# Performance work log

Measured on AMD Instinct MI355X. Metric: run time of the kernel, lower is better.

## Reference

```python
import jax, jax.numpy as jnp
import numpy as np

N, E = 40000, 640000
DIN, HID, H = 512, 128, 4
C = HID  # per-head channels; H*C == 512 == DIN
BN_EPS = 1e-5


def setup_inputs() -> dict:
    key = jax.random.key(0)
    ks = jax.random.split(key, 32)
    sc = 0.05
    d = {}
    d["x"] = jax.random.normal(ks[0], (N, DIN), jnp.float32)
    d["edge_index"] = jax.random.randint(ks[1], (2, E), 0, N)
    i = 2
    for l in (1, 2, 3):
        d[f"W{l}"] = jax.random.normal(ks[i], (DIN, H * C), jnp.float32) * sc; i += 1
        d[f"as{l}"] = jax.random.normal(ks[i], (H, C), jnp.float32) * sc; i += 1
        d[f"ad{l}"] = jax.random.normal(ks[i], (H, C), jnp.float32) * sc; i += 1
        d[f"b{l}"] = jnp.zeros((H * C,), jnp.float32)
        d[f"g{l}"] = jnp.ones((H * C,), jnp.float32)
        d[f"be{l}"] = jnp.zeros((H * C,), jnp.float32)
    d["Wg1"] = jax.random.normal(ks[i], (H * C, HID), jnp.float32) * sc; i += 1
    d["bg1"] = jnp.zeros((HID,), jnp.float32)
    d["Wg2"] = jax.random.normal(ks[i], (HID, 1), jnp.float32) * sc; i += 1
    d["bg2"] = jnp.zeros((1,), jnp.float32)
    d["Wf1"] = jax.random.normal(ks[i], (H * C, HID), jnp.float32) * sc; i += 1
    d["bf1"] = jnp.zeros((HID,), jnp.float32)
    d["Wf2"] = jax.random.normal(ks[i], (HID, HID), jnp.float32) * sc; i += 1
    d["bf2"] = jnp.zeros((HID,), jnp.float32)
    d["Wp"] = jax.random.normal(ks[i], (HID + H * C, HID), jnp.float32) * sc; i += 1
    d["bp"] = jnp.zeros((HID,), jnp.float32)
    return d


def _gat(x, src, dst, W, a_s, a_d, b):
    # PyG GATConv (concat=True, negative_slope=0.2, self-loops already in src/dst)
    n = x.shape[0]
    h = (x @ W).reshape(n, H, C)                      # [N,H,C]
    es = jnp.einsum('nhc,hc->nh', h, a_s)             # alpha_src per node
    ed = jnp.einsum('nhc,hc->nh', h, a_d)             # alpha_dst per node
    e = jax.nn.leaky_relu(es[src] + ed[dst], 0.2)     # [Etot,H]
    m = jax.ops.segment_max(e, dst, num_segments=n)   # softmax over incoming edges
    ex = jnp.exp(e - m[dst])
    s = jax.ops.segment_sum(ex, dst, num_segments=n)
    w = ex / (s[dst] + 1e-16)                         # [Etot,H]
    out = jax.ops.segment_sum(w[:, :, None] * h[src], dst, num_segments=n)
    return out.reshape(n, H * C) + b


def _bn(x, g, b):
    mu = x.mean(0)
    var = x.var(0)
    return (x - mu) * jax.lax.rsqrt(var + BN_EPS) * g + b


def reference(x, edge_index,
              W1, as1, ad1, b1, g1, be1,
              W2, as2, ad2, b2, g2, be2,
              W3, as3, ad3, b3, g3, be3,
              Wg1, bg1, Wg2, bg2, Wf1, bf1, Wf2, bf2, Wp, bp):
    n = x.shape[0]
    loops = jnp.arange(n)
    src = jnp.concatenate([edge_index[0], loops])
    dst = jnp.concatenate([edge_index[1], loops])

    h = jax.nn.leaky_relu(_bn(_gat(x, src, dst, W1, as1, ad1, b1), g1, be1), 0.2)
    h_res = h
    h = jax.nn.leaky_relu(_bn(_gat(h, src, dst, W2, as2, ad2, b2), g2, be2), 0.2) + h_res
    h_res = h
    h = jax.nn.leaky_relu(_bn(_gat(h, src, dst, W3, as3, ad3, b3), g3, be3), 0.2) + h_res

    attn_scores = (jnp.tanh(h @ Wg1 + bg1) @ Wg2 + bg2)[:, 0]   # [N]
    attn_w = jax.nn.softmax(attn_scores)                        # softmax over all nodes
    feat = jax.nn.relu(h @ Wf1 + bf1) @ Wf2 + bf2               # [N,HID]
    gated = (attn_w[:, None] * feat).sum(0)                     # [HID]
    global_pooled = h.mean(0, keepdims=True)                    # batch=None -> one graph
    combined = jnp.concatenate([gated[None, :], global_pooled], axis=-1)  # [1,640]
    out = (combined @ Wp + bp)[0]                               # [HID]
    return out, attn_scores
```

## Files before the change

kernel.cpp:

```cpp
#include <hip/hip_runtime.h>
#include <math.h>

#define N_NODES 40000
#define M_PAD   40064
#define N_EDGES 640000
#define ETOT    (N_EDGES + N_NODES)
#define DINC    512
#define NHEAD   4
#define CHD     128
#define BN_EPS  1e-5f

typedef __attribute__((ext_vector_type(8))) short bf16x8;
typedef __attribute__((ext_vector_type(4))) float f32x4;

static __device__ __forceinline__ float lrelu(float x) { return x > 0.f ? x : 0.2f * x; }

static __device__ __forceinline__ unsigned short f2b(float f) {
    union { float f; unsigned int u; } v; v.f = f;
    unsigned int r = (v.u + 0x7fff + ((v.u >> 16) & 1)) >> 16;
    return (unsigned short)r;
}
static __device__ __forceinline__ float b2f(unsigned short b) {
    union { unsigned int u; float f; } v; v.u = ((unsigned int)b) << 16;
    return v.f;
}
static __device__ __forceinline__ float lo16(unsigned int u) {
    union { unsigned int u; float f; } v; v.u = u << 16; return v.f;
}
static __device__ __forceinline__ float hi16(unsigned int u) {
    union { unsigned int u; float f; } v; v.u = u & 0xffff0000u; return v.f;
}

static __device__ __forceinline__ void fma8(float* acc, uint4 hv, float wgt) {
    acc[0] += wgt * lo16(hv.x); acc[1] += wgt * hi16(hv.x);
    acc[2] += wgt * lo16(hv.y); acc[3] += wgt * hi16(hv.y);
    acc[4] += wgt * lo16(hv.z); acc[5] += wgt * hi16(hv.z);
    acc[6] += wgt * lo16(hv.w); acc[7] += wgt * hi16(hv.w);
}

#define GLDS16(g, l) __builtin_amdgcn_global_load_lds( \
    (__attribute__((address_space(1))) void*)(g),      \
    (__attribute__((address_space(3))) void*)(l), 16, 0, 0)

#define CVTX_BLK 10000
__global__ __launch_bounds__(256) void k_prep(const float4* __restrict__ xin,
                                              uint4* __restrict__ xb,
                                              uint4* __restrict__ curb,
                                              uint4* __restrict__ cnt4) {
    int bid = blockIdx.x;
    int tid = threadIdx.x;
    if (bid < CVTX_BLK) {
        size_t i = (size_t)bid * 256 + tid;
        float4 a = xin[i * 2], b = xin[i * 2 + 1];
        uint4 o;
        o.x = (unsigned)f2b(a.x) | ((unsigned)f2b(a.y) << 16);
        o.y = (unsigned)f2b(a.z) | ((unsigned)f2b(a.w) << 16);
        o.z = (unsigned)f2b(b.x) | ((unsigned)f2b(b.y) << 16);
        o.w = (unsigned)f2b(b.z) | ((unsigned)f2b(b.w) << 16);
        xb[i] = o;
    } else if (bid < CVTX_BLK + 16) {
        int i = (bid - CVTX_BLK) * 256 + tid;
        xb[(size_t)N_NODES * DINC / 8 + i] = make_uint4(0, 0, 0, 0);
    } else if (bid < CVTX_BLK + 32) {
        int i = (bid - CVTX_BLK - 16) * 256 + tid;
        curb[(size_t)N_NODES * DINC / 8 + i] = make_uint4(0, 0, 0, 0);
    } else {
        int i = (bid - CVTX_BLK - 32) * 256 + tid;
        if (i < N_NODES / 4) cnt4[i] = make_uint4(0, 0, 0, 0);
    }
}

__global__ __launch_bounds__(256) void k_cvtw_all(const float* __restrict__ W1, unsigned short* __restrict__ T1,
                                                  const float* __restrict__ W2, unsigned short* __restrict__ T2,
                                                  const float* __restrict__ W3, unsigned short* __restrict__ T3,
                                                  const float* __restrict__ Wg1, const float* __restrict__ Wf1,
                                                  unsigned short* __restrict__ Wct) {
    int idx = blockIdx.x * 256 + threadIdx.x;
    const float* W; unsigned short* T; int Nn;
    if (idx < 262144)            { W = W1; T = T1; Nn = 512; }
    else if (idx < 524288)       { W = W2; T = T2; Nn = 512; idx -= 262144; }
    else if (idx < 786432)       { W = W3; T = T3; Nn = 512; idx -= 524288; }
    else if (idx < 851968)       { W = Wg1; T = Wct; Nn = 128; idx -= 786432; }
    else                         { W = Wf1; T = Wct + 65536; Nn = 128; idx -= 851968; }
    int k = idx / Nn, n = idx % Nn;
    T[(size_t)n * 512 + k] = f2b(W[idx]);
}

__global__ void k_degree(const int* __restrict__ ei, int* __restrict__ cnt) {
    int e = blockIdx.x * 256 + threadIdx.x;
    if (e < ETOT) {
        int dst = (e < N_EDGES) ? ei[N_EDGES + e] : (e - N_EDGES);
        atomicAdd(&cnt[dst], 1);
    }
}

__global__ __launch_bounds__(64) void k_scan1(const int* __restrict__ deg, int* __restrict__ bsum) {
    int lane = threadIdx.x;
    int v = deg[blockIdx.x * 64 + lane];
#pragma unroll
    for (int off = 32; off; off >>= 1) v += __shfl_xor(v, off);
    if (lane == 0) bsum[blockIdx.x] = v;
}

__global__ __launch_bounds__(64) void k_scan23(const int* __restrict__ deg, const int* __restrict__ bsum,
                                               int* __restrict__ rowptr, int* __restrict__ cnt) {
    int b = blockIdx.x, lane = threadIdx.x;
    int pre = 0;
    for (int i = lane; i < b; i += 64) pre += bsum[i];
#pragma unroll
    for (int off = 32; off; off >>= 1) pre += __shfl_xor(pre, off);
    int i = b * 64 + lane;
    int v = deg[i];
    int inc = v;
#pragma unroll
    for (int off = 1; off < 64; off <<= 1) {
        int t = __shfl_up(inc, off);
        if (lane >= off) inc += t;
    }
    rowptr[i] = pre + inc - v;
    cnt[i] = 0;
    if (b == 624 && lane == 63) rowptr[N_NODES] = ETOT;
}

__global__ void k_fill(const int* __restrict__ ei, const int* __restrict__ rowptr,
                       int* __restrict__ cnt, int* __restrict__ csr_src) {
    int e = blockIdx.x * 256 + threadIdx.x;
    if (e < ETOT) {
        int src, dst;
        if (e < N_EDGES) { src = ei[e]; dst = ei[N_EDGES + e]; }
        else             { src = e - N_EDGES; dst = src; }
        int pos = rowptr[dst] + atomicAdd(&cnt[dst], 1);
        csr_src[pos] = src;
    }
}

template<int CBF16, int EPI>
__global__ __launch_bounds__(256) void k_gemm_mfma(const unsigned short* __restrict__ A,
                                                   const unsigned short* __restrict__ Bt,
                                                   void* __restrict__ Cout,
                                                   int Nn, int K, int nbn,
                                                   const float* __restrict__ p1,
                                                   const float* __restrict__ p2,
                                                   float* __restrict__ p3,
                                                   float* __restrict__ p4,
                                                   const float* __restrict__ p5,
                                                   const float* __restrict__ p6) {
    __shared__ alignas(16) unsigned short As[128 * 64];
    __shared__ alignas(16) unsigned short Bs[128 * 64];
    const int tid  = threadIdx.x;
    const int wv   = tid >> 6;
    const int lane = tid & 63;
    const int bm = (blockIdx.x / nbn) * 128;
    const int bn = (blockIdx.x % nbn) * 128;
    const int wm = (wv >> 1) * 64;
    const int wn = (wv & 1) * 64;

    const int srow = lane >> 3;
    const int scol = (((lane & 7) ^ srow) * 8);
    const size_t a_base = (size_t)(bm + wv * 32 + srow) * K + scol;
    const size_t b_base = (size_t)(bn + wv * 32 + srow) * K + scol;

    f32x4 acc[4][4] = {};

    for (int k0 = 0; k0 < K; k0 += 64) {
#pragma unroll
        for (int q = 0; q < 4; ++q)
            GLDS16(A + a_base + (size_t)q * 8 * K + k0, &As[(wv * 32 + q * 8) * 64]);
#pragma unroll
        for (int q = 0; q < 4; ++q)
            GLDS16(Bt + b_base + (size_t)q * 8 * K + k0, &Bs[(wv * 32 + q * 8) * 64]);
        __syncthreads();

        const int r0 = lane & 15;
#pragma unroll
        for (int ks = 0; ks < 2; ++ks) {
            const int c = ks * 4 + (lane >> 4);
            bf16x8 af[4], bfr[4];
#pragma unroll
            for (int i = 0; i < 4; ++i) {
                int row = wm + i * 16 + r0;
                af[i] = *(const bf16x8*)&As[row * 64 + ((c ^ (row & 7)) * 8)];
            }
#pragma unroll
            for (int j = 0; j < 4; ++j) {
                int row = wn + j * 16 + r0;
                bfr[j] = *(const bf16x8*)&Bs[row * 64 + ((c ^ (row & 7)) * 8)];
            }
#pragma unroll
            for (int i = 0; i < 4; ++i)
#pragma unroll
                for (int j = 0; j < 4; ++j)
                    acc[i][j] = __builtin_amdgcn_mfma_f32_16x16x32_bf16(af[i], bfr[j], acc[i][j], 0, 0, 0);
        }
        __syncthreads();
    }

    const int crow0 = bm + wm + (lane >> 4) * 4;
    const int ccol  = bn + wn + (lane & 15);

    if (EPI != 2) {
#pragma unroll
        for (int i = 0; i < 4; ++i)
#pragma unroll
            for (int j = 0; j < 4; ++j)
#pragma unroll
                for (int r = 0; r < 4; ++r) {
                    size_t off = (size_t)(crow0 + i * 16 + r) * Nn + ccol + j * 16;
                    if (CBF16) ((unsigned short*)Cout)[off] = f2b(acc[i][j][r]);
                    else       ((float*)Cout)[off] = acc[i][j][r];
                }
    }

    if (EPI == 1) {
        const int head = bn >> 7;
        float asv[4], adv[4];
#pragma unroll
        for (int j = 0; j < 4; ++j) {
            int cc = head * CHD + wn + j * 16 + (lane & 15);
            asv[j] = p1[cc];
            adv[j] = p2[cc];
        }
        float* sE = (float*)As;
        sE[tid] = 0.f;
        __syncthreads();
#pragma unroll
        for (int i = 0; i < 4; ++i)
#pragma unroll
            for (int r = 0; r < 4; ++r) {
                float e = acc[i][0][r] * asv[0] + acc[i][1][r] * asv[1]
                        + acc[i][2][r] * asv[2] + acc[i][3][r] * asv[3];
                float d = acc[i][0][r] * adv[0] + acc[i][1][r] * adv[1]
                        + acc[i][2][r] * adv[2] + acc[i][3][r] * adv[3];
#pragma unroll
                for (int off = 8; off; off >>= 1) {
                    e += __shfl_xor(e, off);
                    d += __shfl_xor(d, off);
                }
                if ((lane & 15) == 0) {
                    int rloc = wm + i * 16 + (lane >> 4) * 4 + r;
                    atomicAdd(&sE[rloc], e);
                    atomicAdd(&sE[128 + rloc], d);
                }
            }
        __syncthreads();
        if (tid < 128) {
            p3[(size_t)(bm + tid) * NHEAD + head] = sE[tid];
            p4[(size_t)(bm + tid) * NHEAD + head] = sE[128 + tid];
        }
    }

    if (EPI == 2) {
        if (bn == 0) {
            float wgv[4], bgv[4];
#pragma unroll
            for (int j = 0; j < 4; ++j) {
                int cc = wn + j * 16 + (lane & 15);
                bgv[j] = p1[cc];
                wgv[j] = p2[cc];
            }
            float* sE = (float*)As;
            sE[tid] = 0.f;
            __syncthreads();
#pragma unroll
            for (int i = 0; i < 4; ++i)
#pragma unroll
                for (int r = 0; r < 4; ++r) {
                    float e = tanhf(acc[i][0][r] + bgv[0]) * wgv[0]
                            + tanhf(acc[i][1][r] + bgv[1]) * wgv[1]
                            + tanhf(acc[i][2][r] + bgv[2]) * wgv[2]
                            + tanhf(acc[i][3][r] + bgv[3]) * wgv[3];
#pragma unroll
                    for (int off = 8; off; off >>= 1) e += __shfl_xor(e, off);
                    if ((lane & 15) == 0)
                        atomicAdd(&sE[wm + i * 16 + (lane >> 4) * 4 + r], e);
                }
            __syncthreads();
            if (tid < 128) p3[bm + tid] = sE[tid] + p5[0];
        } else {
#pragma unroll
            for (int j = 0; j < 4; ++j) {
                int colF = wn + j * 16 + (lane & 15);
                float bv = p6[colF];
#pragma unroll
                for (int i = 0; i < 4; ++i)
#pragma unroll
                    for (int r = 0; r < 4; ++r)
                        p4[(size_t)(crow0 + i * 16 + r) * 128 + colF] =
                            fmaxf(acc[i][j][r] + bv, 0.f);
            }
        }
    }
}

__global__ __launch_bounds__(256) void k_wts(const float4* __restrict__ es4,
                                             const float4* __restrict__ ed4,
                                             const int* __restrict__ rowptr,
                                             const int* __restrict__ csr_src,
                                             float4* __restrict__ wbuf4,
                                             float4* __restrict__ inv4,
                                             float* __restrict__ stats) {
    if (blockIdx.x == 0)
        for (int q = threadIdx.x; q < DINC * 2; q += 256) stats[q] = 0.f;
    int n = blockIdx.x * 4 + (threadIdx.x >> 6);
    int lane = threadIdx.x & 63;
    int start = rowptr[n], end = rowptr[n + 1];
    float4 edn = ed4[n];
    float4 mx = make_float4(-1e30f, -1e30f, -1e30f, -1e30f);
    for (int j0 = start; j0 < end; j0 += 64) {
        int j = j0 + lane;
        if (j < end) {
            int s = csr_src[j];
            float4 e = es4[s];
            mx.x = fmaxf(mx.x, lrelu(e.x + edn.x));
            mx.y = fmaxf(mx.y, lrelu(e.y + edn.y));
            mx.z = fmaxf(mx.z, lrelu(e.z + edn.z));
            mx.w = fmaxf(mx.w, lrelu(e.w + edn.w));
        }
    }
#pragma unroll
    for (int off = 32; off; off >>= 1) {
        mx.x = fmaxf(mx.x, __shfl_xor(mx.x, off));
        mx.y = fmaxf(mx.y, __shfl_xor(mx.y, off));
        mx.z = fmaxf(mx.z, __shfl_xor(mx.z, off));
        mx.w = fmaxf(mx.w, __shfl_xor(mx.w, off));
    }
    float4 sum = make_float4(0.f, 0.f, 0.f, 0.f);
    for (int j0 = start; j0 < end; j0 += 64) {
        int j = j0 + lane;
        if (j < end) {
            int s = csr_src[j];
            float4 e = es4[s];
            float4 ex;
            ex.x = __expf(lrelu(e.x + edn.x) - mx.x);
            ex.y = __expf(lrelu(e.y + edn.y) - mx.y);
            ex.z = __expf(lrelu(e.z + edn.z) - mx.z);
            ex.w = __expf(lrelu(e.w + edn.w) - mx.w);
            wbuf4[j] = ex;
            sum.x += ex.x; sum.y += ex.y; sum.z += ex.z; sum.w += ex.w;
        }
    }
#pragma unroll
    for (int off = 32; off; off >>= 1) {
        sum.x += __shfl_xor(sum.x, off);
        sum.y += __shfl_xor(sum.y, off);
        sum.z += __shfl_xor(sum.z, off);
        sum.w += __shfl_xor(sum.w, off);
    }
    if (lane == 0) {
        float4 iv;
        iv.x = 1.f / (sum.x + 1e-16f);
        iv.y = 1.f / (sum.y + 1e-16f);
        iv.z = 1.f / (sum.z + 1e-16f);
        iv.w = 1.f / (sum.w + 1e-16f);
        inv4[n] = iv;
    }
}

__global__ __launch_bounds__(256) void k_agg(const unsigned short* __restrict__ hb,
                                             const int* __restrict__ rowptr,
                                             const int* __restrict__ csr_src,
                                             const float* __restrict__ wbuf,
                                             const float* __restrict__ invp,
                                             unsigned short* __restrict__ aggb) {
    __shared__ float part[4][512];
    const int n = blockIdx.x;
    const int tid = threadIdx.x;
    const int grp = tid >> 6;
    const int lane = tid & 63;
    const int head = lane >> 4;
    const int start = rowptr[n], end = rowptr[n + 1];

    float acc[8] = {};
    int j = start + grp;
    int s_n = 0; float w_n = 0.f;
    if (j < end) { s_n = csr_src[j]; w_n = wbuf[j * 4 + head]; }
    while (j < end) {
        int s = s_n; float wgt = w_n;
        int j2 = j + 4;
        if (j2 < end) { s_n = csr_src[j2]; w_n = wbuf[j2 * 4 + head]; }
        uint4 hv = *(const uint4*)&hb[(size_t)s * DINC + lane * 8];
        fma8(acc, hv, wgt);
        j = j2;
    }
    *(float4*)&part[grp][lane * 8]     = make_float4(acc[0], acc[1], acc[2], acc[3]);
    *(float4*)&part[grp][lane * 8 + 4] = make_float4(acc[4], acc[5], acc[6], acc[7]);
    __syncthreads();
    const int c = tid * 2;
    float v0 = part[0][c] + part[1][c] + part[2][c] + part[3][c];
    float v1 = part[0][c + 1] + part[1][c + 1] + part[2][c + 1] + part[3][c + 1];
    float iv = invp[(n << 2) + (c >> 7)];
    v0 *= iv; v1 *= iv;
    unsigned int o = (unsigned)f2b(v0) | ((unsigned)f2b(v1) << 16);
    *(unsigned int*)&aggb[(size_t)n * DINC + c] = o;
}

__global__ __launch_bounds__(256) void k_bn_stats(const unsigned short* __restrict__ aggb,
                                                  float* __restrict__ stats) {
    int tid = threadIdx.x;
    int row0 = blockIdx.x * 64;
    int c0 = tid * 2;
    float s0 = 0, q0 = 0, s1 = 0, q1 = 0;
    for (int r = row0; r < row0 + 64; ++r) {
        unsigned int hv = *(const unsigned int*)&aggb[(size_t)r * DINC + c0];
        float v0 = lo16(hv), v1 = hi16(hv);
        s0 += v0; q0 += v0 * v0;
        s1 += v1; q1 += v1 * v1;
    }
    atomicAdd(&stats[c0], s0);
    atomicAdd(&stats[c0 + 1], s1);
    atomicAdd(&stats[DINC + c0], q0);
    atomicAdd(&stats[DINC + c0 + 1], q1);
}

__global__ __launch_bounds__(256) void k_bn_act(const unsigned short* __restrict__ aggb,
                                                const float* __restrict__ stats,
                                                const float* __restrict__ g,
                                                const float* __restrict__ be,
                                                unsigned short* __restrict__ curb,
                                                int res) {
    size_t idx = (size_t)blockIdx.x * 256 + threadIdx.x;
    int c8 = ((int)(idx & 63)) * 8;
    uint4 v = *(const uint4*)&aggb[idx * 8];
    float xv[8] = { lo16(v.x), hi16(v.x), lo16(v.y), hi16(v.y),
                    lo16(v.z), hi16(v.z), lo16(v.w), hi16(v.w) };
#pragma unroll
    for (int q = 0; q < 8; ++q) {
        int c = c8 + q;
        float mu = stats[c] * (1.f / N_NODES);
        float var = stats[DINC + c] * (1.f / N_NODES) - mu * mu;
        float A = g[c] * rsqrtf(var + BN_EPS);
        float B = be[c] - mu * A;
        xv[q] = lrelu(xv[q] * A + B);
    }
    if (res) {
        uint4 r = *(const uint4*)&curb[idx * 8];
        xv[0] += lo16(r.x); xv[1] += hi16(r.x);
        xv[2] += lo16(r.y); xv[3] += hi16(r.y);
        xv[4] += lo16(r.z); xv[5] += hi16(r.z);
        xv[6] += lo16(r.w); xv[7] += hi16(r.w);
    }
    uint4 o;
    o.x = (unsigned)f2b(xv[0]) | ((unsigned)f2b(xv[1]) << 16);
    o.y = (unsigned)f2b(xv[2]) | ((unsigned)f2b(xv[3]) << 16);
    o.z = (unsigned)f2b(xv[4]) | ((unsigned)f2b(xv[5]) << 16);
    o.w = (unsigned)f2b(xv[6]) | ((unsigned)f2b(xv[7]) << 16);
    *(uint4*)&curb[idx * 8] = o;
}

__global__ __launch_bounds__(1024) void k_softmax(const float* __restrict__ scores, float* __restrict__ sm,
                                                  float* __restrict__ vbuf, float* __restrict__ pooled) {
    __shared__ float red[16];
    int tid = threadIdx.x, lane = tid & 63, wv = tid >> 6;
    if (tid < 128) vbuf[tid] = 0.f;
    if (tid < DINC) pooled[tid] = 0.f;
    float m = -1e30f;
    for (int i = tid; i < N_NODES; i += 1024) m = fmaxf(m, scores[i]);
#pragma unroll
    for (int off = 32; off; off >>= 1) m = fmaxf(m, __shfl_xor(m, off));
    if (lane == 0) red[wv] = m;
    __syncthreads();
    float mall = red[0];
    for (int i = 1; i < 16; ++i) mall = fmaxf(mall, red[i]);
    __syncthreads();
    float s = 0.f;
    for (int i = tid; i < N_NODES; i += 1024) s += expf(scores[i] - mall);
#pragma unroll
    for (int off = 32; off; off >>= 1) s += __shfl_xor(s, off);
    if (lane == 0) red[wv] = s;
    __syncthreads();
    if (tid == 0) {
        float tot = 0.f;
        for (int i = 0; i < 16; ++i) tot += red[i];
        sm[0] = mall; sm[1] = tot;
    }
}

__global__ __launch_bounds__(640) void k_vpool(const float* __restrict__ Fb,
                                               const unsigned short* __restrict__ hb,
                                               const float* __restrict__ scores,
                                               const float* __restrict__ sm,
                                               float* __restrict__ v,
                                               float* __restrict__ pooled) {
    int tid = threadIdx.x;
    int row0 = blockIdx.x * 64;
    float mall = sm[0];
    float invS = 1.f / sm[1];
    if (tid < 128) {
        float acc = 0.f;
        for (int r = row0; r < row0 + 64; ++r) {
            float w = expf(scores[r] - mall) * invS;
            acc += w * Fb[(size_t)r * 128 + tid];
        }
        atomicAdd(&v[tid], acc);
    } else {
        int c = tid - 128;
        float acc = 0.f;
        for (int r = row0; r < row0 + 64; ++r) acc += b2f(hb[(size_t)r * DINC + c]);
        atomicAdd(&pooled[c], acc * (1.f / N_NODES));
    }
}

__global__ __launch_bounds__(128) void k_final(const float* __restrict__ v,
                                               const float* __restrict__ pooled,
                                               const float* __restrict__ Wf2,
                                               const float* __restrict__ bf2,
                                               const float* __restrict__ Wp,
                                               const float* __restrict__ bp,
                                               float* __restrict__ out) {
    __shared__ float sg[128];
    int o = threadIdx.x;
    float g = bf2[o];
    for (int k = 0; k < 128; ++k) g += v[k] * Wf2[k * 128 + o];
    sg[o] = g;
    __syncthreads();
    float acc = bp[o];
    for (int c = 0; c < 128; ++c) acc += sg[c] * Wp[c * 128 + o];
    for (int j = 0; j < 512; ++j) acc += pooled[j] * Wp[(128 + j) * 128 + o];
    out[o] = acc;
}

extern "C" void kernel_launch(void* const* d_in, const int* in_sizes, int n_in,
                              void* d_out, int out_size, void* d_ws, size_t ws_size,
                              hipStream_t stream) {
    const float* x  = (const float*)d_in[0];
    const int*   ei = (const int*)d_in[1];
    const float* Wg1 = (const float*)d_in[20];
    const float* bg1 = (const float*)d_in[21];
    const float* Wg2 = (const float*)d_in[22];
    const float* bg2 = (const float*)d_in[23];
    const float* Wf1 = (const float*)d_in[24];
    const float* bf1 = (const float*)d_in[25];
    const float* Wf2 = (const float*)d_in[26];
    const float* bf2 = (const float*)d_in[27];
    const float* Wp  = (const float*)d_in[28];
    const float* bp  = (const float*)d_in[29];
    float* out = (float*)d_out;

    char* base = (char*)d_ws;
    size_t off = 0;
    auto take = [&](size_t nbytes) -> char* {
        char* p = base + off;
        off += (nbytes + 255) & ~(size_t)255;
        return p;
    };
    unsigned short* hb   = (unsigned short*)take((size_t)M_PAD * DINC * 2);
    unsigned short* curb = (unsigned short*)take((size_t)M_PAD * DINC * 2);
    unsigned short* xb   = (unsigned short*)take((size_t)M_PAD * DINC * 2);
    unsigned short* aggb = (unsigned short*)take((size_t)M_PAD * DINC * 2);
    float* Fb    = (float*)take((size_t)M_PAD * 128 * 4);
    float* es    = (float*)take((size_t)M_PAD * NHEAD * 4);
    float* ed    = (float*)take((size_t)M_PAD * NHEAD * 4);
    float* wbuf  = (float*)take((size_t)ETOT * NHEAD * 4);
    float* invp  = (float*)take((size_t)N_NODES * NHEAD * 4);
    int*   rowptr= (int*)take((size_t)(N_NODES + 1) * 4);
    int*   cnt   = (int*)take((size_t)N_NODES * 4);
    int*   csr   = (int*)take((size_t)ETOT * 4);
    int*   bsum  = (int*)take(625 * 4);
    float* stats = (float*)take(DINC * 2 * 4);
    float* sm    = (float*)take(2 * 4);
    float* vbuf  = (float*)take(128 * 4);
    float* pooled= (float*)take(DINC * 4);
    unsigned short* Wt1  = (unsigned short*)take((size_t)DINC * DINC * 2);
    unsigned short* Wt2  = (unsigned short*)take((size_t)DINC * DINC * 2);
    unsigned short* Wt3  = (unsigned short*)take((size_t)DINC * DINC * 2);
    unsigned short* Wct  = (unsigned short*)take((size_t)256 * DINC * 2);

    k_prep<<<CVTX_BLK + 32 + 40, 256, 0, stream>>>((const float4*)x, (uint4*)xb,
                                                   (uint4*)curb, (uint4*)cnt);
    k_cvtw_all<<<3584, 256, 0, stream>>>((const float*)d_in[2], Wt1,
                                         (const float*)d_in[8], Wt2,
                                         (const float*)d_in[14], Wt3,
                                         Wg1, Wf1, Wct);
    k_degree<<<(ETOT + 255) / 256, 256, 0, stream>>>(ei, cnt);
    k_scan1<<<625, 64, 0, stream>>>(cnt, bsum);
    k_scan23<<<625, 64, 0, stream>>>(cnt, bsum, rowptr, cnt);
    k_fill<<<(ETOT + 255) / 256, 256, 0, stream>>>(ei, rowptr, cnt, csr);

    const unsigned short* Wts[3] = {Wt1, Wt2, Wt3};
    const unsigned short* in = xb;
    for (int l = 0; l < 3; ++l) {
        const float* as_ = (const float*)d_in[2 + l * 6 + 1];
        const float* ad_ = (const float*)d_in[2 + l * 6 + 2];
        const float* g   = (const float*)d_in[2 + l * 6 + 4];
        const float* be  = (const float*)d_in[2 + l * 6 + 5];

        k_gemm_mfma<1, 1><<<(M_PAD / 128) * (DINC / 128), 256, 0, stream>>>(
            in, Wts[l], hb, DINC, DINC, DINC / 128, as_, ad_, es, ed, nullptr, nullptr);
        k_wts<<<N_NODES / 4, 256, 0, stream>>>((const float4*)es, (const float4*)ed, rowptr, csr,
                                               (float4*)wbuf, (float4*)invp, stats);
        k_agg<<<N_NODES, 256, 0, stream>>>(hb, rowptr, csr, wbuf, invp, aggb);
        k_bn_stats<<<N_NODES / 64, 256, 0, stream>>>(aggb, stats);
        k_bn_act<<<(N_NODES * (DINC / 8)) / 256, 256, 0, stream>>>(aggb, stats, g, be, curb, l > 0 ? 1 : 0);
        in = curb;
    }

    float* scores = out + 128;
    k_gemm_mfma<0, 2><<<(M_PAD / 128) * 2, 256, 0, stream>>>(
        curb, Wct, nullptr, 256, DINC, 2, bg1, Wg2, scores, Fb, bg2, bf1);

    k_softmax<<<1, 1024, 0, stream>>>(scores, sm, vbuf, pooled);
    k_vpool<<<N_NODES / 64, 640, 0, stream>>>(Fb, curb, scores, sm, vbuf, pooled);
    k_final<<<1, 128, 0, stream>>>(vbuf, pooled, Wf2, bf2, Wp, bp, out);
}
```

Baseline: 891.6 us.

## Fuse edge softmax weight computation into aggregation kernel and drop max pass

Removes the separate k_wts kernel. Each aggregation block now computes exp of the leaky-relu edge logits directly into shared memory and accumulates per-head sums with shared atomics, eliminating the global wbuf/invp round trip and one launch per layer. The max-subtraction pass is dropped, relying on softmax shift invariance, which risks overflow for large logits. The pooling kernel is also narrowed to 384 threads, each reading two bf16 columns per load.

```diff
diff --git a/kernel.cpp b/kernel.cpp
--- a/kernel.cpp
+++ b/kernel.cpp
@@ -292,77 +292,17 @@
     }
 }
 
-__global__ __launch_bounds__(256) void k_wts(const float4* __restrict__ es4,
+__global__ __launch_bounds__(256) void k_agg(const unsigned short* __restrict__ hb,
+                                             const float4* __restrict__ es4,
                                              const float4* __restrict__ ed4,
                                              const int* __restrict__ rowptr,
                                              const int* __restrict__ csr_src,
-                                             float4* __restrict__ wbuf4,
-                                             float4* __restrict__ inv4,
+                                             unsigned short* __restrict__ aggb,
                                              float* __restrict__ stats) {
-    if (blockIdx.x == 0)
-        for (int q = threadIdx.x; q < DINC * 2; q += 256) stats[q] = 0.f;
-    int n = blockIdx.x * 4 + (threadIdx.x >> 6);
-    int lane = threadIdx.x & 63;
-    int start = rowptr[n], end = rowptr[n + 1];
-    float4 edn = ed4[n];
-    float4 mx = make_float4(-1e30f, -1e30f, -1e30f, -1e30f);
-    for (int j0 = start; j0 < end; j0 += 64) {
-        int j = j0 + lane;
-        if (j < end) {
-            int s = csr_src[j];
-            float4 e = es4[s];
-            mx.x = fmaxf(mx.x, lrelu(e.x + edn.x));
-            mx.y = fmaxf(mx.y, lrelu(e.y + edn.y));
-            mx.z = fmaxf(mx.z, lrelu(e.z + edn.z));
-            mx.w = fmaxf(mx.w, lrelu(e.w + edn.w));
-        }
-    }
-#pragma unroll
-    for (int off = 32; off; off >>= 1) {
-        mx.x = fmaxf(mx.x, __shfl_xor(mx.x, off));
-        mx.y = fmaxf(mx.y, __shfl_xor(mx.y, off));
-        mx.z = fmaxf(mx.z, __shfl_xor(mx.z, off));
-        mx.w = fmaxf(mx.w, __shfl_xor(mx.w, off));
-    }
-    float4 sum = make_float4(0.f, 0.f, 0.f, 0.f);
-    for (int j0 = start; j0 < end; j0 += 64) {
-        int j = j0 + lane;
-        if (j < end) {
-            int s = csr_src[j];
-            float4 e = es4[s];
-            float4 ex;
-            ex.x = __expf(lrelu(e.x + edn.x) - mx.x);
-            ex.y = __expf(lrelu(e.y + edn.y) - mx.y);
-            ex.z = __expf(lrelu(e.z + edn.z) - mx.z);
-            ex.w = __expf(lrelu(e.w + edn.w) - mx.w);
-            wbuf4[j] = ex;
-            sum.x += ex.x; sum.y += ex.y; sum.z += ex.z; sum.w += ex.w;
-        }
-    }
-#pragma unroll
-    for (int off = 32; off; off >>= 1) {
-        sum.x += __shfl_xor(sum.x, off);
-        sum.y += __shfl_xor(sum.y, off);
-        sum.z += __shfl_xor(sum.z, off);
-        sum.w += __shfl_xor(sum.w, off);
-    }
-    if (lane == 0) {
-        float4 iv;
-        iv.x = 1.f / (sum.x + 1e-16f);
-        iv.y = 1.f / (sum.y + 1e-16f);
-        iv.z = 1.f / (sum.z + 1e-16f);
-        iv.w = 1.f / (sum.w + 1e-16f);
-        inv4[n] = iv;
-    }
-}
-
-__global__ __launch_bounds__(256) void k_agg(const unsigned short* __restrict__ hb,
-                                             const int* __restrict__ rowptr,
-                                             const int* __restrict__ csr_src,
-                                             const float* __restrict__ wbuf,
-                                             const float* __restrict__ invp,
-                                             unsigned short* __restrict__ aggb) {
     __shared__ float part[4][512];
+    __shared__ float4 s_w[256];
+    __shared__ int s_src[256];
+    __shared__ float s_sum[4];
     const int n = blockIdx.x;
     const int tid = threadIdx.x;
     const int grp = tid >> 6;
@@ -370,17 +310,42 @@
     const int head = lane >> 4;
     const int start = rowptr[n], end = rowptr[n + 1];
 
+    if (n == 0)
+        for (int q = tid; q < DINC * 2; q += 256) stats[q] = 0.f;
+    if (tid < 4) s_sum[tid] = 1e-16f;
+    const float4 edn = ed4[n];
+
     float acc[8] = {};
-    int j = start + grp;
-    int s_n = 0; float w_n = 0.f;
-    if (j < end) { s_n = csr_src[j]; w_n = wbuf[j * 4 + head]; }
-    while (j < end) {
-        int s = s_n; float wgt = w_n;
-        int j2 = j + 4;
-        if (j2 < end) { s_n = csr_src[j2]; w_n = wbuf[j2 * 4 + head]; }
-        uint4 hv = *(const uint4*)&hb[(size_t)s * DINC + lane * 8];
-        fma8(acc, hv, wgt);
-        j = j2;
+    for (int base = start; base < end; base += 256) {
+        const int cnt = min(256, end - base);
+        __syncthreads();
+        if (tid < cnt) {
+            int s = csr_src[base + tid];
+            s_src[tid] = s;
+            float4 e = es4[s];
+            float4 ex;
+            ex.x = __expf(lrelu(e.x + edn.x));
+            ex.y = __expf(lrelu(e.y + edn.y));
+            ex.z = __expf(lrelu(e.z + edn.z));
+            ex.w = __expf(lrelu(e.w + edn.w));
+            s_w[tid] = ex;
+            atomicAdd(&s_sum[0], ex.x);
+            atomicAdd(&s_sum[1], ex.y);
+            atomicAdd(&s_sum[2], ex.z);
+            atomicAdd(&s_sum[3], ex.w);
+        }
+        __syncthreads();
+        int i = grp;
+        int s_n = 0; float w_n = 0.f;
+        if (i < cnt) { s_n = s_src[i]; w_n = ((const float*)&s_w[i])[head]; }
+        while (i < cnt) {
+            int s = s_n; float wgt = w_n;
+            int i2 = i + 4;
+            if (i2 < cnt) { s_n = s_src[i2]; w_n = ((const float*)&s_w[i2])[head]; }
+            uint4 hv = *(const uint4*)&hb[(size_t)s * DINC + lane * 8];
+            fma8(acc, hv, wgt);
+            i = i2;
+        }
     }
     *(float4*)&part[grp][lane * 8]     = make_float4(acc[0], acc[1], acc[2], acc[3]);
     *(float4*)&part[grp][lane * 8 + 4] = make_float4(acc[4], acc[5], acc[6], acc[7]);
@@ -388,7 +353,7 @@
     const int c = tid * 2;
     float v0 = part[0][c] + part[1][c] + part[2][c] + part[3][c];
     float v1 = part[0][c + 1] + part[1][c + 1] + part[2][c + 1] + part[3][c + 1];
-    float iv = invp[(n << 2) + (c >> 7)];
+    float iv = 1.f / s_sum[tid >> 6];
     v0 *= iv; v1 *= iv;
     unsigned int o = (unsigned)f2b(v0) | ((unsigned)f2b(v1) << 16);
     *(unsigned int*)&aggb[(size_t)n * DINC + c] = o;
@@ -475,7 +440,7 @@
     }
 }
 
-__global__ __launch_bounds__(640) void k_vpool(const float* __restrict__ Fb,
+__global__ __launch_bounds__(384) void k_vpool(const float* __restrict__ Fb,
                                                const unsigned short* __restrict__ hb,
                                                const float* __restrict__ scores,
                                                const float* __restrict__ sm,
@@ -493,10 +458,14 @@
         }
         atomicAdd(&v[tid], acc);
     } else {
-        int c = tid - 128;
-        float acc = 0.f;
-        for (int r = row0; r < row0 + 64; ++r) acc += b2f(hb[(size_t)r * DINC + c]);
-        atomicAdd(&pooled[c], acc * (1.f / N_NODES));
+        int c = (tid - 128) * 2;
+        float a0 = 0.f, a1 = 0.f;
+        for (int r = row0; r < row0 + 64; ++r) {
+            unsigned int hv = *(const unsigned int*)&hb[(size_t)r * DINC + c];
+            a0 += lo16(hv); a1 += hi16(hv);
+        }
+        atomicAdd(&pooled[c], a0 * (1.f / N_NODES));
+        atomicAdd(&pooled[c + 1], a1 * (1.f / N_NODES));
     }
 }
 
@@ -550,8 +519,6 @@
     float* Fb    = (float*)take((size_t)M_PAD * 128 * 4);
     float* es    = (float*)take((size_t)M_PAD * NHEAD * 4);
     float* ed    = (float*)take((size_t)M_PAD * NHEAD * 4);
-    float* wbuf  = (float*)take((size_t)ETOT * NHEAD * 4);
-    float* invp  = (float*)take((size_t)N_NODES * NHEAD * 4);
     int*   rowptr= (int*)take((size_t)(N_NODES + 1) * 4);
     int*   cnt   = (int*)take((size_t)N_NODES * 4);
     int*   csr   = (int*)take((size_t)ETOT * 4);
@@ -586,9 +553,8 @@
 
         k_gemm_mfma<1, 1><<<(M_PAD / 128) * (DINC / 128), 256, 0, stream>>>(
             in, Wts[l], hb, DINC, DINC, DINC / 128, as_, ad_, es, ed, nullptr, nullptr);
-        k_wts<<<N_NODES / 4, 256, 0, stream>>>((const float4*)es, (const float4*)ed, rowptr, csr,
-                                               (float4*)wbuf, (float4*)invp, stats);
-        k_agg<<<N_NODES, 256, 0, stream>>>(hb, rowptr, csr, wbuf, invp, aggb);
+        k_agg<<<N_NODES, 256, 0, stream>>>(hb, (const float4*)es, (const float4*)ed,
+                                           rowptr, csr, aggb, stats);
         k_bn_stats<<<N_NODES / 64, 256, 0, stream>>>(aggb, stats);
         k_bn_act<<<(N_NODES * (DINC / 8)) / 256, 256, 0, stream>>>(aggb, stats, g, be, curb, l > 0 ? 1 : 0);
         in = curb;
@@ -599,6 +565,6 @@
         curb, Wct, nullptr, 256, DINC, 2, bg1, Wg2, scores, Fb, bg2, bf1);
 
     k_softmax<<<1, 1024, 0, stream>>>(scores, sm, vbuf, pooled);
-    k_vpool<<<N_NODES / 64, 640, 0, stream>>>(Fb, curb, scores, sm, vbuf, pooled);
+    k_vpool<<<N_NODES / 64, 384, 0, stream>>>(Fb, curb, scores, sm, vbuf, pooled);
     k_final<<<1, 128, 0, stream>>>(vbuf, pooled, Wf2, bf2, Wp, bp, out);
 }
```

Result: slower. 919.1 us (+3.1%).
